# Kernel tuning notes

Measured on AMD Instinct MI355X. Metric: run time of the kernel, lower is better.

Reference implementation:

```python
import jax, jax.numpy as jnp
import numpy as np

B, T, C, H = 2, 2048, 1024, 16
D = C // H  # head dim = 64


def setup_inputs() -> dict:
    key = jax.random.key(0)
    ks = jax.random.split(key, 5)
    s = 0.02
    return {
        "x": jax.random.normal(ks[0], (B, T, C), dtype=jnp.float32),
        "W_attn": jax.random.normal(ks[1], (C, 3 * C), dtype=jnp.float32) * s,
        "b_attn": jax.random.normal(ks[2], (3 * C,), dtype=jnp.float32) * s,
        "W_proj": jax.random.normal(ks[3], (C, C), dtype=jnp.float32) * s,
        "b_proj": jax.random.normal(ks[4], (C,), dtype=jnp.float32) * s,
    }


def reference(x, W_attn, b_attn, W_proj, b_proj):
    Bb, Tt, Cc = x.shape
    kqv = x @ W_attn + b_attn                     # [B,T,3C]
    q, k, v = jnp.split(kqv, 3, axis=2)           # each [B,T,C]
    # reshape to heads: [B,H,T,D]
    q = q.reshape(Bb, Tt, H, D).transpose(0, 2, 1, 3)
    k = k.reshape(Bb, Tt, H, D).transpose(0, 2, 1, 3)
    v = v.reshape(Bb, Tt, H, D).transpose(0, 2, 1, 3)
    scale = 1.0 / jnp.sqrt(jnp.float32(D))
    att = jnp.einsum('bhqd,bhkd->bhqk', q, k) * scale  # [B,H,T,T]
    causal = jnp.tril(jnp.ones((Tt, Tt), dtype=bool))
    att = jnp.where(causal[None, None], att, -jnp.inf)
    att = jax.nn.softmax(att, axis=-1)
    y = jnp.einsum('bhqk,bhkd->bhqd', att, v)      # [B,H,T,D]
    y = y.transpose(0, 2, 1, 3).reshape(Bb, Tt, Cc)
    return y @ W_proj + b_proj
```

## Files before the change

kernel.cpp:

```cpp
#include <hip/hip_runtime.h>
#include <hip/hip_bf16.h>
#include <math.h>

typedef __attribute__((ext_vector_type(4))) float f32x4;
typedef __attribute__((ext_vector_type(8))) short short8;
typedef __attribute__((ext_vector_type(4))) short short4v;

__device__ __forceinline__ short f2bf(float f) {
    union { __hip_bfloat16 h; short s; } u;
    u.h = __float2bfloat16(f);
    return u.s;
}

__device__ __forceinline__ f32x4 mfma16(short8 a, short8 b, f32x4 c) {
    return __builtin_amdgcn_mfma_f32_16x16x32_bf16(a, b, c, 0, 0, 0);
}

__global__ __launch_bounds__(256) void cvt_bf16(const float* __restrict__ in,
                                                short* __restrict__ out, int n) {
    int i = (blockIdx.x * 256 + threadIdx.x) * 8;
    if (i >= n) return;
    float4 a = *reinterpret_cast<const float4*>(in + i);
    float4 b = *reinterpret_cast<const float4*>(in + i + 4);
    short8 o;
    o[0] = f2bf(a.x); o[1] = f2bf(a.y); o[2] = f2bf(a.z); o[3] = f2bf(a.w);
    o[4] = f2bf(b.x); o[5] = f2bf(b.y); o[6] = f2bf(b.z); o[7] = f2bf(b.w);
    *reinterpret_cast<short8*>(out + i) = o;
}

__global__ __launch_bounds__(256) void transpose_w(const float* __restrict__ W,
                                                   short* __restrict__ Wt,
                                                   int K, int N) {
    __shared__ float tile[64][68];
    const int k0 = blockIdx.x * 64;
    const int n0 = blockIdx.y * 64;
    const int tid = threadIdx.x;
    #pragma unroll
    for (int i = 0; i < 4; ++i) {
        int c = tid + i * 256;
        int r = c >> 4;
        int col4 = (c & 15) * 4;
        float4 v = *reinterpret_cast<const float4*>(W + (size_t)(k0 + r) * N + n0 + col4);
        tile[r][col4 + 0] = v.x; tile[r][col4 + 1] = v.y;
        tile[r][col4 + 2] = v.z; tile[r][col4 + 3] = v.w;
    }
    __syncthreads();
    #pragma unroll
    for (int i = 0; i < 4; ++i) {
        int c = tid + i * 256;
        int r2 = c >> 4;
        int col4 = (c & 15) * 4;
        short4v o;
        #pragma unroll
        for (int j = 0; j < 4; ++j) o[j] = f2bf(tile[col4 + j][r2]);
        *reinterpret_cast<short4v*>(Wt + (size_t)(n0 + r2) * K + k0 + col4) = o;
    }
}

template<int MODE>
__global__ __launch_bounds__(256) void gemm_bt(const short* __restrict__ A,
                                               const short* __restrict__ Bt,
                                               const float* __restrict__ bias,
                                               void* __restrict__ C,
                                               short* __restrict__ vt,
                                               int M, int N, int K) {
    constexpr int BM = 128, BN = 128, BK = 64, LDP = BK + 8;
    __shared__ short As[BM * LDP];
    __shared__ short Bs[BN * LDP];
    const int tid = threadIdx.x;
    const int lane = tid & 63, wave = tid >> 6;
    const int bm = blockIdx.x * BM, bn = blockIdx.y * BN;
    const int wr = (wave >> 1) * 64, wc = (wave & 1) * 64;
    const int g = lane >> 4, l15 = lane & 15;

    f32x4 acc[4][4] = {};

    for (int k0 = 0; k0 < K; k0 += BK) {
        __syncthreads();
        #pragma unroll
        for (int i = 0; i < 4; ++i) {
            int c = tid + i * 256;
            int r = c >> 3;
            int col = (c & 7) * 8;
            *reinterpret_cast<short8*>(&As[r * LDP + col]) =
                *reinterpret_cast<const short8*>(A + (size_t)(bm + r) * K + k0 + col);
            *reinterpret_cast<short8*>(&Bs[r * LDP + col]) =
                *reinterpret_cast<const short8*>(Bt + (size_t)(bn + r) * K + k0 + col);
        }
        __syncthreads();
        #pragma unroll
        for (int kk = 0; kk < 2; ++kk) {
            short8 af[4], bfr[4];
            #pragma unroll
            for (int m = 0; m < 4; ++m)
                af[m] = *reinterpret_cast<const short8*>(&As[(wr + m * 16 + l15) * LDP + kk * 32 + g * 8]);
            #pragma unroll
            for (int n = 0; n < 4; ++n)
                bfr[n] = *reinterpret_cast<const short8*>(&Bs[(wc + n * 16 + l15) * LDP + kk * 32 + g * 8]);
            #pragma unroll
            for (int m = 0; m < 4; ++m)
                #pragma unroll
                for (int n = 0; n < 4; ++n)
                    acc[m][n] = mfma16(af[m], bfr[n], acc[m][n]);
        }
    }

    #pragma unroll
    for (int m = 0; m < 4; ++m)
        #pragma unroll
        for (int n = 0; n < 4; ++n) {
            int gc = bn + wc + n * 16 + l15;
            float bv = bias[gc];
            int gr0 = bm + wr + m * 16 + g * 4;
            if (MODE == 0) {
                #pragma unroll
                for (int r = 0; r < 4; ++r)
                    reinterpret_cast<float*>(C)[(size_t)(gr0 + r) * N + gc] = acc[m][n][r] + bv;
            } else {
                if (gc < 2048) {
                    float sc = (gc < 1024) ? 0.125f : 1.0f;
                    short* qkp = reinterpret_cast<short*>(C);
                    #pragma unroll
                    for (int r = 0; r < 4; ++r)
                        qkp[(size_t)(gr0 + r) * 2048 + gc] = f2bf((acc[m][n][r] + bv) * sc);
                } else {
                    int cv = gc - 2048;
                    int bb = gr0 >> 11;
                    int t0 = gr0 & 2047;
                    short4v o;
                    #pragma unroll
                    for (int r = 0; r < 4; ++r) o[r] = f2bf(acc[m][n][r] + bv);
                    *reinterpret_cast<short4v*>(&vt[((size_t)(bb << 10) + cv) * 2048 + t0]) = o;
                }
            }
        }
}


template<int NMAX, int KKMAX, bool MASK>
__device__ __forceinline__ void tile_step(const short* __restrict__ Kl,
                                          const short* __restrict__ Vl,
                                          short* Ps, int l15, int g,
                                          const short8 (&qf)[2][2],
                                          f32x4 (&oacc)[2][4],
                                          f32x4 (&lacc)[2],
                                          float (&mst)[2][4],
                                          int rowbase, int colbase,
                                          short8 ones) {
    f32x4 sacc[2][NMAX + 1];
    #pragma unroll
    for (int m = 0; m < 2; ++m)
        #pragma unroll
        for (int n = 0; n <= NMAX; ++n) sacc[m][n] = f32x4{0.f, 0.f, 0.f, 0.f};
    __builtin_amdgcn_s_setprio(1);
    #pragma unroll
    for (int kk = 0; kk < 2; ++kk)
        #pragma unroll
        for (int n = 0; n <= NMAX; ++n) {
            short8 kf = *reinterpret_cast<const short8*>(Kl + (size_t)n * 16 * 2048 + kk * 32);
            sacc[0][n] = mfma16(qf[0][kk], kf, sacc[0][n]);
            sacc[1][n] = mfma16(qf[1][kk], kf, sacc[1][n]);
        }
    __builtin_amdgcn_s_setprio(0);

    short8 vf[KKMAX + 1][4];
    #pragma unroll
    for (int kk = 0; kk <= KKMAX; ++kk)
        #pragma unroll
        for (int nd = 0; nd < 4; ++nd)
            vf[kk][nd] = *reinterpret_cast<const short8*>(Vl + (size_t)nd * 16 * 2048 + kk * 32);

    if (MASK) {
        #pragma unroll
        for (int m = 0; m < 2; ++m)
            #pragma unroll
            for (int n = 0; n <= NMAX; ++n)
                #pragma unroll
                for (int r = 0; r < 4; ++r) {
                    int row = rowbase + m * 16 + r;
                    int col = colbase + n * 16;
                    if (col > row) sacc[m][n][r] = -INFINITY;
                }
    }

    #pragma unroll
    for (int m = 0; m < 2; ++m)
        #pragma unroll
        for (int r = 0; r < 4; ++r) {
            float rm = sacc[m][0][r];
            #pragma unroll
            for (int n = 1; n <= NMAX; ++n) rm = fmaxf(rm, sacc[m][n][r]);
            #pragma unroll
            for (int w = 1; w < 16; w <<= 1) rm = fmaxf(rm, __shfl_xor(rm, w));
            float mn = fmaxf(mst[m][r], rm);
            float corr = __expf(mst[m][r] - mn);
            mst[m][r] = mn;
            #pragma unroll
            for (int n = 0; n <= NMAX; ++n) {
                float p = __expf(sacc[m][n][r] - mn);
                Ps[(g * 4 + m * 16 + r) * 72 + n * 16 + l15] = f2bf(p);
            }
            lacc[m][r] *= corr;
            #pragma unroll
            for (int nd = 0; nd < 4; ++nd) oacc[m][nd][r] *= corr;
        }

    __builtin_amdgcn_s_setprio(1);
    #pragma unroll
    for (int kk = 0; kk <= KKMAX; ++kk) {
        short8 pa0 = *reinterpret_cast<const short8*>(&Ps[l15 * 72 + kk * 32 + g * 8]);
        short8 pa1 = *reinterpret_cast<const short8*>(&Ps[(16 + l15) * 72 + kk * 32 + g * 8]);
        #pragma unroll
        for (int nd = 0; nd < 4; ++nd) {
            oacc[0][nd] = mfma16(pa0, vf[kk][nd], oacc[0][nd]);
            oacc[1][nd] = mfma16(pa1, vf[kk][nd], oacc[1][nd]);
        }
        lacc[0] = mfma16(pa0, ones, lacc[0]);
        lacc[1] = mfma16(pa1, ones, lacc[1]);
    }
    __builtin_amdgcn_s_setprio(0);
}

__global__ __launch_bounds__(64) void attn_kernel(const short* __restrict__ qk,
                                                  const short* __restrict__ vt,
                                                  short* __restrict__ yatt) {
    constexpr int T = 2048;
    __shared__ short Ps[32 * 72];

    const int lane = threadIdx.x & 63;
    const int g = lane >> 4, l15 = lane & 15;

    const int bid = blockIdx.x;
    const int xcd = bid & 7;
    const int idx = bid >> 3;
    const int grp = xcd * 4 + (idx >> 6);
    const int h = grp & 15, b = grp >> 4;
    const int qt = 63 - (idx & 63);
    const int qs = qt * 32;

    const size_t baseQ = (size_t)b * T * 2048 + (size_t)h * 64;
    const short* Kl = qk + baseQ + 1024 + (size_t)l15 * 2048 + g * 8;
    const short* Vl = vt + ((size_t)b * 1024 + (size_t)h * 64) * 2048 + (size_t)l15 * 2048 + g * 8;

    short8 ones;
    #pragma unroll
    for (int i = 0; i < 8; ++i) ones[i] = (short)0x3F80;

    short8 qf[2][2];
    #pragma unroll
    for (int m = 0; m < 2; ++m)
        #pragma unroll
        for (int kk = 0; kk < 2; ++kk)
            qf[m][kk] = *reinterpret_cast<const short8*>(
                qk + baseQ + (size_t)(qs + m * 16 + l15) * 2048 + kk * 32 + g * 8);

    f32x4 oacc[2][4] = {};
    f32x4 lacc[2] = {};
    float mst[2][4];
    #pragma unroll
    for (int m = 0; m < 2; ++m)
        #pragma unroll
        for (int r = 0; r < 4; ++r) mst[m][r] = -INFINITY;

    const int rowbase = qs + g * 4;
    int colbase = l15;
    const int jd = qt >> 1;

    const short* Klj = Kl;
    const short* Vlj = Vl;
    for (int j = 0; j < jd; ++j) {
        tile_step<3, 1, false>(Klj, Vlj, Ps, l15, g, qf, oacc, lacc, mst, rowbase, colbase, ones);
        Klj += 64 * 2048;
        Vlj += 64;
        colbase += 64;
    }
    if (qt & 1)
        tile_step<3, 1, true>(Klj, Vlj, Ps, l15, g, qf, oacc, lacc, mst, rowbase, colbase, ones);
    else
        tile_step<1, 0, true>(Klj, Vlj, Ps, l15, g, qf, oacc, lacc, mst, rowbase, colbase, ones);

    #pragma unroll
    for (int m = 0; m < 2; ++m)
        #pragma unroll
        for (int r = 0; r < 4; ++r) {
            float rl = 1.0f / lacc[m][r];
            int row = qs + m * 16 + g * 4 + r;
            #pragma unroll
            for (int nd = 0; nd < 4; ++nd) {
                int col = nd * 16 + l15;
                yatt[((size_t)b * T + row) * 1024 + h * 64 + col] = f2bf(oacc[m][nd][r] * rl);
            }
        }
}

extern "C" void kernel_launch(void* const* d_in, const int* in_sizes, int n_in,
                              void* d_out, int out_size, void* d_ws, size_t ws_size,
                              hipStream_t stream) {
    constexpr int B = 2, T = 2048, C = 1024;
    constexpr int M = B * T;
    constexpr int N1 = 3 * C;
    constexpr int K = C;

    const float* x      = (const float*)d_in[0];
    const float* W_attn = (const float*)d_in[1];
    const float* b_attn = (const float*)d_in[2];
    const float* W_proj = (const float*)d_in[3];
    const float* b_proj = (const float*)d_in[4];
    float* out = (float*)d_out;

    char* ws = (char*)d_ws;
    short* x_bf    = (short*)(ws);
    short* Wt_attn = (short*)(ws + 8388608);
    short* Wt_proj = (short*)(ws + 14680064);
    short* qk      = (short*)(ws + 16777216);
    short* vt      = (short*)(ws + 33554432);
    short* yatt    = (short*)(ws + 41943040);

    cvt_bf16<<<dim3(M * K / (256 * 8)), 256, 0, stream>>>(x, x_bf, M * K);
    transpose_w<<<dim3(K / 64, N1 / 64), 256, 0, stream>>>(W_attn, Wt_attn, K, N1);
    transpose_w<<<dim3(K / 64, C / 64), 256, 0, stream>>>(W_proj, Wt_proj, K, C);

    gemm_bt<1><<<dim3(M / 128, N1 / 128), 256, 0, stream>>>(x_bf, Wt_attn, b_attn, qk, vt, M, N1, K);
    attn_kernel<<<dim3(2048), 64, 0, stream>>>(qk, vt, yatt);
    gemm_bt<0><<<dim3(M / 128, C / 128), 256, 0, stream>>>(yatt, Wt_proj, b_proj, out, nullptr, M, C, C);
}
```

Baseline: 184.4 us.

## Split long causal attention rows into KV chunks with log-sum-exp merge kernel

Long query tiles are split across two or three KV chunks of up to twelve steps each, so the causal triangle is spread over more, evenly sized workgroups. Each partial result is written in bf16 along with its log-sum-exp, and a new merge kernel combines them into the attention output. The aim is to cut the tail imbalance from the longest query tiles. The cost is an extra launch, extra global traffic for the partials, some bf16 rounding of the partials, and reuse of the x_bf workspace region for the partial buffer.

```diff
diff --git a/kernel.cpp b/kernel.cpp
--- a/kernel.cpp
+++ b/kernel.cpp
@@ -10,6 +10,12 @@
     union { __hip_bfloat16 h; short s; } u;
     u.h = __float2bfloat16(f);
     return u.s;
+}
+
+__device__ __forceinline__ float bf2f(short s) {
+    union { float f; unsigned u; } x;
+    x.u = ((unsigned)(unsigned short)s) << 16;
+    return x.f;
 }
 
 __device__ __forceinline__ f32x4 mfma16(short8 a, short8 b, f32x4 c) {
@@ -221,9 +227,10 @@
     __builtin_amdgcn_s_setprio(0);
 }
 
-__global__ __launch_bounds__(64) void attn_kernel(const short* __restrict__ qk,
-                                                  const short* __restrict__ vt,
-                                                  short* __restrict__ yatt) {
+__global__ __launch_bounds__(64) void attn_chunk(const short* __restrict__ qk,
+                                                 const short* __restrict__ vt,
+                                                 short* __restrict__ yatt,
+                                                 short* __restrict__ part) {
     constexpr int T = 2048;
     __shared__ short Ps[32 * 72];
 
@@ -233,11 +240,22 @@
     const int bid = blockIdx.x;
     const int xcd = bid & 7;
     const int idx = bid >> 3;
-    const int grp = xcd * 4 + (idx >> 6);
+    const int g4 = idx / 120;
+    const int c = 119 - (idx - g4 * 120);
+    const int grp = xcd * 4 + g4;
     const int h = grp & 15, b = grp >> 4;
-    const int qt = 63 - (idx & 63);
+    int qt, ch;
+    if (c < 24)      { qt = c; ch = 0; }
+    else if (c < 72) { int t = c - 24; qt = 24 + (t >> 1); ch = t & 1; }
+    else             { int t = c - 72; int q3 = t / 3; qt = 48 + q3; ch = t - q3 * 3; }
+
+    const int nsteps = (qt >> 1) + 1;
+    const int s0 = ch * 12;
+    const int s1 = (s0 + 12 < nsteps) ? s0 + 12 : nsteps;
+    const bool hasdiag = (s1 == nsteps);
+    const int nfull = s1 - s0 - (hasdiag ? 1 : 0);
+
     const int qs = qt * 32;
-
     const size_t baseQ = (size_t)b * T * 2048 + (size_t)h * 64;
     const short* Kl = qk + baseQ + 1024 + (size_t)l15 * 2048 + g * 8;
     const short* Vl = vt + ((size_t)b * 1024 + (size_t)h * 64) * 2048 + (size_t)l15 * 2048 + g * 8;
@@ -263,34 +281,95 @@
         for (int r = 0; r < 4; ++r) mst[m][r] = -INFINITY;
 
     const int rowbase = qs + g * 4;
-    int colbase = l15;
-    const int jd = qt >> 1;
-
-    const short* Klj = Kl;
-    const short* Vlj = Vl;
-    for (int j = 0; j < jd; ++j) {
+    int colbase = l15 + s0 * 64;
+    const short* Klj = Kl + (size_t)s0 * 64 * 2048;
+    const short* Vlj = Vl + s0 * 64;
+
+    for (int j = 0; j < nfull; ++j) {
         tile_step<3, 1, false>(Klj, Vlj, Ps, l15, g, qf, oacc, lacc, mst, rowbase, colbase, ones);
         Klj += 64 * 2048;
         Vlj += 64;
         colbase += 64;
     }
-    if (qt & 1)
-        tile_step<3, 1, true>(Klj, Vlj, Ps, l15, g, qf, oacc, lacc, mst, rowbase, colbase, ones);
-    else
-        tile_step<1, 0, true>(Klj, Vlj, Ps, l15, g, qf, oacc, lacc, mst, rowbase, colbase, ones);
-
-    #pragma unroll
-    for (int m = 0; m < 2; ++m)
-        #pragma unroll
-        for (int r = 0; r < 4; ++r) {
-            float rl = 1.0f / lacc[m][r];
-            int row = qs + m * 16 + g * 4 + r;
-            #pragma unroll
-            for (int nd = 0; nd < 4; ++nd) {
-                int col = nd * 16 + l15;
-                yatt[((size_t)b * T + row) * 1024 + h * 64 + col] = f2bf(oacc[m][nd][r] * rl);
+    if (hasdiag) {
+        if (qt & 1)
+            tile_step<3, 1, true>(Klj, Vlj, Ps, l15, g, qf, oacc, lacc, mst, rowbase, colbase, ones);
+        else
+            tile_step<1, 0, true>(Klj, Vlj, Ps, l15, g, qf, oacc, lacc, mst, rowbase, colbase, ones);
+    }
+
+    if (qt < 24) {
+        #pragma unroll
+        for (int m = 0; m < 2; ++m)
+            #pragma unroll
+            for (int r = 0; r < 4; ++r) {
+                float rl = 1.0f / lacc[m][r];
+                int row = qs + m * 16 + g * 4 + r;
+                #pragma unroll
+                for (int nd = 0; nd < 4; ++nd) {
+                    int col = nd * 16 + l15;
+                    yatt[((size_t)b * T + row) * 1024 + h * 64 + col] = f2bf(oacc[m][nd][r] * rl);
+                }
             }
-        }
+    } else {
+        const int p = grp * 96 + ((qt < 48) ? (qt - 24) * 2 + ch : 48 + (qt - 48) * 3 + ch);
+        short* Pp = part + (size_t)p * 2112;
+        #pragma unroll
+        for (int m = 0; m < 2; ++m)
+            #pragma unroll
+            for (int r = 0; r < 4; ++r) {
+                float rl = 1.0f / lacc[m][r];
+                int rloc = m * 16 + g * 4 + r;
+                #pragma unroll
+                for (int nd = 0; nd < 4; ++nd)
+                    Pp[rloc * 64 + nd * 16 + l15] = f2bf(oacc[m][nd][r] * rl);
+            }
+        if (l15 == 0) {
+            float* Lp = reinterpret_cast<float*>(Pp + 2048);
+            #pragma unroll
+            for (int m = 0; m < 2; ++m)
+                #pragma unroll
+                for (int r = 0; r < 4; ++r)
+                    Lp[m * 16 + g * 4 + r] = mst[m][r] + __logf(lacc[m][r]);
+        }
+    }
+}
+
+__global__ __launch_bounds__(64) void attn_merge(const short* __restrict__ part,
+                                                 short* __restrict__ yatt) {
+    const int bid = blockIdx.x;
+    const int xcd = bid & 7;
+    const int idx = bid >> 3;
+    const int g4 = idx / 40;
+    const int qt = 24 + (idx - g4 * 40);
+    const int grp = xcd * 4 + g4;
+    const int h = grp & 15, b = grp >> 4;
+    const int nc = (qt < 48) ? 2 : 3;
+    const int p0 = grp * 96 + ((qt < 48) ? (qt - 24) * 2 : 48 + (qt - 48) * 3);
+    const int d = threadIdx.x & 63;
+
+    const short* P0 = part + (size_t)p0 * 2112;
+    #pragma unroll 4
+    for (int r = 0; r < 32; ++r) {
+        float lse[3], mx;
+        lse[0] = reinterpret_cast<const float*>(P0 + 2048)[r];
+        lse[1] = reinterpret_cast<const float*>(P0 + 2112 + 2048)[r];
+        mx = fmaxf(lse[0], lse[1]);
+        if (nc == 3) {
+            lse[2] = reinterpret_cast<const float*>(P0 + 2 * 2112 + 2048)[r];
+            mx = fmaxf(mx, lse[2]);
+        }
+        float w0 = __expf(lse[0] - mx);
+        float w1 = __expf(lse[1] - mx);
+        float wsum = w0 + w1;
+        float acc = w0 * bf2f(P0[r * 64 + d]) + w1 * bf2f(P0[2112 + r * 64 + d]);
+        if (nc == 3) {
+            float w2 = __expf(lse[2] - mx);
+            wsum += w2;
+            acc += w2 * bf2f(P0[2 * 2112 + r * 64 + d]);
+        }
+        yatt[((size_t)b * 2048 + qt * 32 + r) * 1024 + h * 64 + d] = f2bf(acc / wsum);
+    }
 }
 
 extern "C" void kernel_launch(void* const* d_in, const int* in_sizes, int n_in,
@@ -315,12 +394,14 @@
     short* qk      = (short*)(ws + 16777216);
     short* vt      = (short*)(ws + 33554432);
     short* yatt    = (short*)(ws + 41943040);
+    short* part    = (short*)(ws);
 
     cvt_bf16<<<dim3(M * K / (256 * 8)), 256, 0, stream>>>(x, x_bf, M * K);
     transpose_w<<<dim3(K / 64, N1 / 64), 256, 0, stream>>>(W_attn, Wt_attn, K, N1);
     transpose_w<<<dim3(K / 64, C / 64), 256, 0, stream>>>(W_proj, Wt_proj, K, C);
 
     gemm_bt<1><<<dim3(M / 128, N1 / 128), 256, 0, stream>>>(x_bf, Wt_attn, b_attn, qk, vt, M, N1, K);
-    attn_kernel<<<dim3(2048), 64, 0, stream>>>(qk, vt, yatt);
+    attn_chunk<<<dim3(3840), 64, 0, stream>>>(qk, vt, yatt, part);
+    attn_merge<<<dim3(1280), 64, 0, stream>>>(part, yatt);
     gemm_bt<0><<<dim3(M / 128, C / 128), 256, 0, stream>>>(yatt, Wt_proj, b_proj, out, nullptr, M, C, C);
 }
```

New measurement: 192.4 us. 1.04x slower.
